# Kernel optimization log

Measured on AMD Instinct MI355X. Metric: run time of the kernel, lower is better.

Reference implementation:

```python
import jax, jax.numpy as jnp
import numpy as np

N_EMBD = 512
HEAD_SIZE = 64
B, T = 256, 256


def setup_inputs() -> dict:
    key = jax.random.key(0)
    ks = jax.random.split(key, 7)
    s = 1.0 / np.sqrt(N_EMBD)
    return {
        "x": jax.random.normal(ks[0], (B, T, N_EMBD), dtype=jnp.float32),
        "Wk": jax.random.uniform(ks[1], (N_EMBD, HEAD_SIZE), jnp.float32, -s, s),
        "bk": jax.random.uniform(ks[2], (HEAD_SIZE,), jnp.float32, -s, s),
        "Wq": jax.random.uniform(ks[3], (N_EMBD, HEAD_SIZE), jnp.float32, -s, s),
        "bq": jax.random.uniform(ks[4], (HEAD_SIZE,), jnp.float32, -s, s),
        "Wv": jax.random.uniform(ks[5], (N_EMBD, HEAD_SIZE), jnp.float32, -s, s),
        "bv": jax.random.uniform(ks[6], (HEAD_SIZE,), jnp.float32, -s, s),
    }


def reference(x, Wk, bk, Wq, bq, Wv, bv):
    # Single-head causal self-attention (dropout = identity in eval mode).
    Bq, Tq, C = x.shape
    k = x @ Wk + bk        # [B, T, H]
    q = x @ Wq + bq        # [B, T, H]
    v = x @ Wv + bv        # [B, T, H]
    scale = 1.0 / jnp.sqrt(jnp.asarray(k.shape[-1], x.dtype))
    scores = jnp.einsum('bth,bsh->bts', q, k) * scale  # [B, T, T]
    causal = jnp.tril(jnp.ones((Tq, Tq), dtype=bool))
    scores = jnp.where(causal, scores, -jnp.inf)
    attn = jax.nn.softmax(scores, axis=-1)
    return jnp.einsum('bts,bsh->bth', attn, v)  # [B, T, H]
```

## Files before the change

kernel.cpp:

```cpp
#include <hip/hip_runtime.h>
#include <stdint.h>

typedef __attribute__((ext_vector_type(8))) short bf16x8;
typedef __attribute__((ext_vector_type(4))) float f32x4;

#if __has_builtin(__builtin_amdgcn_exp2f)
#define EXP2F(x) __builtin_amdgcn_exp2f(x)
#else
#define EXP2F(x) exp2f(x)
#endif

__device__ __forceinline__ short f2bf(float f) {
    union { float f; uint32_t u; } c; c.f = f;
    return (short)((c.u + 0x7fffu + ((c.u >> 16) & 1u)) >> 16);
}

__global__ void prep_kernel(const float* __restrict__ Wk, const float* __restrict__ bk,
                            const float* __restrict__ Wq, const float* __restrict__ bq,
                            const float* __restrict__ Wv, const float* __restrict__ bv,
                            short* __restrict__ Wt2g, float* __restrict__ bcat) {
    const int col = blockIdx.x;
    const float* W; const float* bb; int c0;
    if (col < 64)       { W = Wk; bb = bk; c0 = col; }
    else if (col < 128) { W = Wq; bb = bq; c0 = col - 64; }
    else                { W = Wv; bb = bv; c0 = col - 128; }
    for (int c = threadIdx.x; c < 512; c += blockDim.x)
        Wt2g[(c >> 5) * (192 * 32) + col * 32 + (c & 31)] = f2bf(W[(size_t)c * 64 + c0]);
    if (threadIdx.x == 0) bcat[col] = bb[c0];
}

#define PSTR 40

__global__ __launch_bounds__(512, 2) void fused_kernel(
    const float* __restrict__ x, const short* __restrict__ Wt2g,
    const float* __restrict__ bcat, float* __restrict__ out) {
    extern __shared__ __align__(16) char smem[];
    short* Ks  = (short*)smem;
    short* Qs  = (short*)(smem + 32768);
    short* Vts = (short*)(smem + 65536);
    short* Ps  = (short*)(smem + 98304);

    const int tid = threadIdx.x;
    const int wave = tid >> 6, lane = tid & 63;
    const int quad = lane >> 4, l16 = lane & 15;
    const int b = blockIdx.x;
    const int ta = wave, tb = 15 - wave;

    f32x4 acc[2][12];
#pragma unroll
    for (int m = 0; m < 2; m++)
#pragma unroll
        for (int i = 0; i < 12; i++) acc[m][i] = (f32x4){0.f, 0.f, 0.f, 0.f};

    const float* xA0 = x + ((size_t)b * 256 + ta * 16 + l16) * 512 + quad * 8;
    const float* xA1 = x + ((size_t)b * 256 + tb * 16 + l16) * 512 + quad * 8;

    f32x4 p00 = *(const f32x4*)xA0, p01 = *(const f32x4*)(xA0 + 4);
    f32x4 p10 = *(const f32x4*)xA1, p11 = *(const f32x4*)(xA1 + 4);

    for (int kc = 0; kc < 16; kc++) {
        bf16x8 a0, a1;
#pragma unroll
        for (int i = 0; i < 4; i++) { a0[i] = f2bf(p00[i]); a0[4 + i] = f2bf(p01[i]); }
#pragma unroll
        for (int i = 0; i < 4; i++) { a1[i] = f2bf(p10[i]); a1[4 + i] = f2bf(p11[i]); }
        if (kc < 15) {
            p00 = *(const f32x4*)(xA0 + (kc + 1) * 32);
            p01 = *(const f32x4*)(xA0 + (kc + 1) * 32 + 4);
            p10 = *(const f32x4*)(xA1 + (kc + 1) * 32);
            p11 = *(const f32x4*)(xA1 + (kc + 1) * 32 + 4);
        }
        const short* wkc = Wt2g + kc * 6144 + l16 * 32 + quad * 8;
#pragma unroll
        for (int nt = 0; nt < 12; nt++) {
            bf16x8 bfrag = *(const bf16x8*)(wkc + nt * 512);
            acc[0][nt] = __builtin_amdgcn_mfma_f32_16x16x32_bf16(a0, bfrag, acc[0][nt], 0, 0, 0);
            acc[1][nt] = __builtin_amdgcn_mfma_f32_16x16x32_bf16(a1, bfrag, acc[1][nt], 0, 0, 0);
        }
    }

#pragma unroll
    for (int m = 0; m < 2; m++) {
        const int t = m ? tb : ta;
#pragma unroll
        for (int nt = 0; nt < 12; nt++) {
            const int col = nt * 16 + l16;
            const float bias = bcat[col];
            const int h = col & 63;
#pragma unroll
            for (int r = 0; r < 4; r++) {
                const short v = f2bf(acc[m][nt][r] + bias);
                const int row = t * 16 + quad * 4 + r;
                if (nt < 4)
                    Ks[row * 64 + (((h >> 3) ^ (row & 7)) << 3) + (h & 7)] = v;
                else if (nt < 8)
                    Qs[row * 64 + (((h >> 3) ^ (row & 7)) << 3) + (h & 7)] = v;
                else
                    Vts[h * 256 + (((row >> 3) ^ (h & 7)) << 3) + (row & 7)] = v;
            }
        }
    }
    __syncthreads();

    const float sc2 = 0.125f * 1.44269504088896340736f;
    short* myP = Ps + wave * (16 * PSTR);

#pragma unroll
    for (int ti = 0; ti < 2; ti++) {
        const int t = ti ? tb : ta;
        const int qrow = t * 16 + l16;
        const int sw = l16 & 7;
        bf16x8 qf0 = *(const bf16x8*)&Qs[qrow * 64 + ((quad ^ sw) << 3)];
        bf16x8 qf1 = *(const bf16x8*)&Qs[qrow * 64 + (((4 + quad) ^ sw) << 3)];

        f32x4 St[16];
#pragma unroll
        for (int i = 0; i < 16; i++) St[i] = (f32x4){0.f, 0.f, 0.f, 0.f};
#pragma unroll
        for (int nt = 0; nt < 16; nt++) if (nt <= t) {
            const int krow = nt * 16 + l16;
            bf16x8 kf0 = *(const bf16x8*)&Ks[krow * 64 + ((quad ^ sw) << 3)];
            bf16x8 kf1 = *(const bf16x8*)&Ks[krow * 64 + (((4 + quad) ^ sw) << 3)];
            St[nt] = __builtin_amdgcn_mfma_f32_16x16x32_bf16(qf0, kf0, St[nt], 0, 0, 0);
            St[nt] = __builtin_amdgcn_mfma_f32_16x16x32_bf16(qf1, kf1, St[nt], 0, 0, 0);
        }

        const int rowq = t * 16 + quad * 4;
        float mx[4], ls[4];
#pragma unroll
        for (int r = 0; r < 4; r++) mx[r] = -3.0e38f;
#pragma unroll
        for (int nt = 0; nt < 16; nt++) if (nt <= t) {
            const int cs = nt * 16 + l16;
#pragma unroll
            for (int r = 0; r < 4; r++) {
                float s = (cs <= rowq + r) ? St[nt][r] * sc2 : -3.0e38f;
                St[nt][r] = s;
                mx[r] = fmaxf(mx[r], s);
            }
        }
#pragma unroll
        for (int d = 1; d < 16; d <<= 1)
#pragma unroll
            for (int r = 0; r < 4; r++)
                mx[r] = fmaxf(mx[r], __shfl_xor(mx[r], d, 64));
#pragma unroll
        for (int r = 0; r < 4; r++) ls[r] = 0.f;
#pragma unroll
        for (int nt = 0; nt < 16; nt++) if (nt <= t) {
#pragma unroll
            for (int r = 0; r < 4; r++) {
                float p = EXP2F(St[nt][r] - mx[r]);
                St[nt][r] = p;
                ls[r] += p;
            }
        }
#pragma unroll
        for (int d = 1; d < 16; d <<= 1)
#pragma unroll
            for (int r = 0; r < 4; r++)
                ls[r] += __shfl_xor(ls[r], d, 64);

        f32x4 O[4];
#pragma unroll
        for (int i = 0; i < 4; i++) O[i] = (f32x4){0.f, 0.f, 0.f, 0.f};
        const int nch = (t + 2) >> 1;
#pragma unroll
        for (int c2 = 0; c2 < 8; c2++) if (c2 < nch) {
#pragma unroll
            for (int t2i = 0; t2i < 2; t2i++) {
                const int nt = c2 * 2 + t2i;
#pragma unroll
                for (int r = 0; r < 4; r++)
                    myP[(quad * 4 + r) * PSTR + t2i * 16 + l16] = f2bf(St[nt][r]);
            }
            bf16x8 pf = *(const bf16x8*)&myP[l16 * PSTR + quad * 8];
#pragma unroll
            for (int ht = 0; ht < 4; ht++) {
                const int h = ht * 16 + l16;
                bf16x8 vf = *(const bf16x8*)&Vts[h * 256 + ((((c2 * 4 + quad)) ^ (h & 7)) << 3)];
                O[ht] = __builtin_amdgcn_mfma_f32_16x16x32_bf16(pf, vf, O[ht], 0, 0, 0);
            }
        }

        float rls[4];
#pragma unroll
        for (int r = 0; r < 4; r++) rls[r] = 1.0f / ls[r];
#pragma unroll
        for (int ht = 0; ht < 4; ht++)
#pragma unroll
            for (int r = 0; r < 4; r++)
                out[((size_t)b * 256 + rowq + r) * 64 + ht * 16 + l16] = O[ht][r] * rls[r];
    }
}

extern "C" void kernel_launch(void* const* d_in, const int* in_sizes, int n_in,
                              void* d_out, int out_size, void* d_ws, size_t ws_size,
                              hipStream_t stream) {
    const float* x  = (const float*)d_in[0];
    const float* Wk = (const float*)d_in[1];
    const float* bk = (const float*)d_in[2];
    const float* Wq = (const float*)d_in[3];
    const float* bq = (const float*)d_in[4];
    const float* Wv = (const float*)d_in[5];
    const float* bv = (const float*)d_in[6];
    float* out = (float*)d_out;

    char* ws = (char*)d_ws;
    short* Wt2g = (short*)(ws);
    float* bcat = (float*)(ws + 196608);

    const int smem_bytes = 108544;
    (void)hipFuncSetAttribute((const void*)fused_kernel,
                              hipFuncAttributeMaxDynamicSharedMemorySize, smem_bytes);

    prep_kernel<<<192, 256, 0, stream>>>(Wk, bk, Wq, bq, Wv, bv, Wt2g, bcat);
    fused_kernel<<<256, 512, smem_bytes, stream>>>(x, Wt2g, bcat, out);
}
```

Baseline: 229.6 us.

## Stage x and W via async global-to-LDS double buffering with 16 waves

Moves the QKV projection operands into LDS with asynchronous global_load_lds copies, double-buffered across K chunks, and reads A and B fragments from shared memory instead of registers or global memory. The block grows to 1024 threads so each of 16 waves owns a single 16-row tile, replacing the paired balanced tiles per wave. This targets the latency of global loads in the projection phase. In exchange it adds extra LDS space and a barrier per K chunk, and causal work per wave becomes uneven in the attention phase.

```diff
diff --git a/kernel.cpp b/kernel.cpp
--- a/kernel.cpp
+++ b/kernel.cpp
@@ -13,6 +13,12 @@
 __device__ __forceinline__ short f2bf(float f) {
     union { float f; uint32_t u; } c; c.f = f;
     return (short)((c.u + 0x7fffu + ((c.u >> 16) & 1u)) >> 16);
+}
+
+typedef __attribute__((address_space(1))) void gvoid;
+typedef __attribute__((address_space(3))) void lvoid;
+__device__ __forceinline__ void async_cp16(const void* g, void* l) {
+    __builtin_amdgcn_global_load_lds((gvoid*)g, (lvoid*)l, 16, 0, 0);
 }
 
 __global__ void prep_kernel(const float* __restrict__ Wk, const float* __restrict__ bk,
@@ -31,73 +37,80 @@
 
 #define PSTR 40
 
-__global__ __launch_bounds__(512, 2) void fused_kernel(
+__global__ __launch_bounds__(1024, 4) void fused_kernel(
     const float* __restrict__ x, const short* __restrict__ Wt2g,
     const float* __restrict__ bcat, float* __restrict__ out) {
     extern __shared__ __align__(16) char smem[];
+
+    const int tid = threadIdx.x;
+    const int wave = tid >> 6, lane = tid & 63;
+    const int quad = lane >> 4, l16 = lane & 15;
+    const int b = blockIdx.x;
+    const int t = wave;
+
+    f32x4 acc[12];
+#pragma unroll
+    for (int i = 0; i < 12; i++) acc[i] = (f32x4){0.f, 0.f, 0.f, 0.f};
+
+    const int xr = lane >> 3;
+    const int xsl = lane & 7;
+
+#define STAGE_X(kc, bufp)                                                           \
+    for (int g = 0; g < 2; g++) {                                                   \
+        const int i = wave + g * 16;                                                \
+        const int r = i * 8 + xr;                                                   \
+        const int s = xsl ^ ((r & 3) << 1);                                         \
+        async_cp16(x + ((size_t)b * 256 + r) * 512 + (kc) * 32 + s * 4,             \
+                   smem + (bufp) * 32768 + i * 1024);                               \
+    }
+#define STAGE_W(kc, bufp)                                                           \
+    if (wave < 12) {                                                                \
+        async_cp16(Wt2g + (size_t)(kc) * 6144 + wave * 512 + lane * 8,              \
+                   smem + 65536 + (bufp) * 12288 + wave * 1024);                    \
+    }
+
+    STAGE_X(0, 0)
+    STAGE_W(0, 0)
+    __syncthreads();
+
+    const int axoff = (quad ^ (l16 & 3)) * 8;
+    const int arow = t * 16 + l16;
+    for (int kc = 0; kc < 16; kc++) {
+        const int buf = kc & 1;
+        if (kc < 15) { STAGE_X(kc + 1, buf ^ 1) STAGE_W(kc + 1, buf ^ 1) }
+        const float* xa = (const float*)(smem + buf * 32768) + arow * 32 + axoff;
+        f32x4 u0 = *(const f32x4*)xa, u1 = *(const f32x4*)(xa + 4);
+        bf16x8 a;
+#pragma unroll
+        for (int i = 0; i < 4; i++) { a[i] = f2bf(u0[i]); a[4 + i] = f2bf(u1[i]); }
+        const short* wb = (const short*)(smem + 65536 + buf * 12288);
+#pragma unroll
+        for (int nt = 0; nt < 12; nt++) {
+            bf16x8 bfrag = *(const bf16x8*)&wb[(nt * 16 + l16) * 32 + quad * 8];
+            acc[nt] = __builtin_amdgcn_mfma_f32_16x16x32_bf16(a, bfrag, acc[nt], 0, 0, 0);
+        }
+        __syncthreads();
+    }
+
     short* Ks  = (short*)smem;
     short* Qs  = (short*)(smem + 32768);
     short* Vts = (short*)(smem + 65536);
     short* Ps  = (short*)(smem + 98304);
-
-    const int tid = threadIdx.x;
-    const int wave = tid >> 6, lane = tid & 63;
-    const int quad = lane >> 4, l16 = lane & 15;
-    const int b = blockIdx.x;
-    const int ta = wave, tb = 15 - wave;
-
-    f32x4 acc[2][12];
-#pragma unroll
-    for (int m = 0; m < 2; m++)
-#pragma unroll
-        for (int i = 0; i < 12; i++) acc[m][i] = (f32x4){0.f, 0.f, 0.f, 0.f};
-
-    const float* xA0 = x + ((size_t)b * 256 + ta * 16 + l16) * 512 + quad * 8;
-    const float* xA1 = x + ((size_t)b * 256 + tb * 16 + l16) * 512 + quad * 8;
-
-    f32x4 p00 = *(const f32x4*)xA0, p01 = *(const f32x4*)(xA0 + 4);
-    f32x4 p10 = *(const f32x4*)xA1, p11 = *(const f32x4*)(xA1 + 4);
-
-    for (int kc = 0; kc < 16; kc++) {
-        bf16x8 a0, a1;
-#pragma unroll
-        for (int i = 0; i < 4; i++) { a0[i] = f2bf(p00[i]); a0[4 + i] = f2bf(p01[i]); }
-#pragma unroll
-        for (int i = 0; i < 4; i++) { a1[i] = f2bf(p10[i]); a1[4 + i] = f2bf(p11[i]); }
-        if (kc < 15) {
-            p00 = *(const f32x4*)(xA0 + (kc + 1) * 32);
-            p01 = *(const f32x4*)(xA0 + (kc + 1) * 32 + 4);
-            p10 = *(const f32x4*)(xA1 + (kc + 1) * 32);
-            p11 = *(const f32x4*)(xA1 + (kc + 1) * 32 + 4);
-        }
-        const short* wkc = Wt2g + kc * 6144 + l16 * 32 + quad * 8;
-#pragma unroll
-        for (int nt = 0; nt < 12; nt++) {
-            bf16x8 bfrag = *(const bf16x8*)(wkc + nt * 512);
-            acc[0][nt] = __builtin_amdgcn_mfma_f32_16x16x32_bf16(a0, bfrag, acc[0][nt], 0, 0, 0);
-            acc[1][nt] = __builtin_amdgcn_mfma_f32_16x16x32_bf16(a1, bfrag, acc[1][nt], 0, 0, 0);
-        }
-    }
-
-#pragma unroll
-    for (int m = 0; m < 2; m++) {
-        const int t = m ? tb : ta;
-#pragma unroll
-        for (int nt = 0; nt < 12; nt++) {
-            const int col = nt * 16 + l16;
-            const float bias = bcat[col];
-            const int h = col & 63;
-#pragma unroll
-            for (int r = 0; r < 4; r++) {
-                const short v = f2bf(acc[m][nt][r] + bias);
-                const int row = t * 16 + quad * 4 + r;
-                if (nt < 4)
-                    Ks[row * 64 + (((h >> 3) ^ (row & 7)) << 3) + (h & 7)] = v;
-                else if (nt < 8)
-                    Qs[row * 64 + (((h >> 3) ^ (row & 7)) << 3) + (h & 7)] = v;
-                else
-                    Vts[h * 256 + (((row >> 3) ^ (h & 7)) << 3) + (row & 7)] = v;
-            }
+#pragma unroll
+    for (int nt = 0; nt < 12; nt++) {
+        const int col = nt * 16 + l16;
+        const float bias = bcat[col];
+        const int h = col & 63;
+#pragma unroll
+        for (int r = 0; r < 4; r++) {
+            const short v = f2bf(acc[nt][r] + bias);
+            const int row = t * 16 + quad * 4 + r;
+            if (nt < 4)
+                Ks[row * 64 + (((h >> 3) ^ (row & 7)) << 3) + (h & 7)] = v;
+            else if (nt < 8)
+                Qs[row * 64 + (((h >> 3) ^ (row & 7)) << 3) + (h & 7)] = v;
+            else
+                Vts[h * 256 + (((row >> 3) ^ (h & 7)) << 3) + (row & 7)] = v;
         }
     }
     __syncthreads();
@@ -105,93 +118,91 @@
     const float sc2 = 0.125f * 1.44269504088896340736f;
     short* myP = Ps + wave * (16 * PSTR);
 
-#pragma unroll
-    for (int ti = 0; ti < 2; ti++) {
-        const int t = ti ? tb : ta;
-        const int qrow = t * 16 + l16;
-        const int sw = l16 & 7;
-        bf16x8 qf0 = *(const bf16x8*)&Qs[qrow * 64 + ((quad ^ sw) << 3)];
-        bf16x8 qf1 = *(const bf16x8*)&Qs[qrow * 64 + (((4 + quad) ^ sw) << 3)];
-
-        f32x4 St[16];
-#pragma unroll
-        for (int i = 0; i < 16; i++) St[i] = (f32x4){0.f, 0.f, 0.f, 0.f};
-#pragma unroll
-        for (int nt = 0; nt < 16; nt++) if (nt <= t) {
-            const int krow = nt * 16 + l16;
-            bf16x8 kf0 = *(const bf16x8*)&Ks[krow * 64 + ((quad ^ sw) << 3)];
-            bf16x8 kf1 = *(const bf16x8*)&Ks[krow * 64 + (((4 + quad) ^ sw) << 3)];
-            St[nt] = __builtin_amdgcn_mfma_f32_16x16x32_bf16(qf0, kf0, St[nt], 0, 0, 0);
-            St[nt] = __builtin_amdgcn_mfma_f32_16x16x32_bf16(qf1, kf1, St[nt], 0, 0, 0);
-        }
-
-        const int rowq = t * 16 + quad * 4;
-        float mx[4], ls[4];
-#pragma unroll
-        for (int r = 0; r < 4; r++) mx[r] = -3.0e38f;
-#pragma unroll
-        for (int nt = 0; nt < 16; nt++) if (nt <= t) {
-            const int cs = nt * 16 + l16;
-#pragma unroll
-            for (int r = 0; r < 4; r++) {
-                float s = (cs <= rowq + r) ? St[nt][r] * sc2 : -3.0e38f;
-                St[nt][r] = s;
-                mx[r] = fmaxf(mx[r], s);
-            }
-        }
-#pragma unroll
-        for (int d = 1; d < 16; d <<= 1)
+    const int qrow = t * 16 + l16;
+    const int sw = l16 & 7;
+    bf16x8 qf0 = *(const bf16x8*)&Qs[qrow * 64 + ((quad ^ sw) << 3)];
+    bf16x8 qf1 = *(const bf16x8*)&Qs[qrow * 64 + (((4 + quad) ^ sw) << 3)];
+
+    f32x4 St[16];
+#pragma unroll
+    for (int i = 0; i < 16; i++) St[i] = (f32x4){0.f, 0.f, 0.f, 0.f};
+#pragma unroll
+    for (int nt = 0; nt < 16; nt++) if (nt <= t) {
+        const int krow = nt * 16 + l16;
+        bf16x8 kf0 = *(const bf16x8*)&Ks[krow * 64 + ((quad ^ sw) << 3)];
+        bf16x8 kf1 = *(const bf16x8*)&Ks[krow * 64 + (((4 + quad) ^ sw) << 3)];
+        St[nt] = __builtin_amdgcn_mfma_f32_16x16x32_bf16(qf0, kf0, St[nt], 0, 0, 0);
+        St[nt] = __builtin_amdgcn_mfma_f32_16x16x32_bf16(qf1, kf1, St[nt], 0, 0, 0);
+    }
+
+    const int rowq = t * 16 + quad * 4;
+    float mx[4], ls[4];
+#pragma unroll
+    for (int r = 0; r < 4; r++) mx[r] = -3.0e38f;
+#pragma unroll
+    for (int nt = 0; nt < 16; nt++) if (nt <= t) {
+        const int cs = nt * 16 + l16;
+#pragma unroll
+        for (int r = 0; r < 4; r++) {
+            float s = (cs <= rowq + r) ? St[nt][r] * sc2 : -3.0e38f;
+            St[nt][r] = s;
+            mx[r] = fmaxf(mx[r], s);
+        }
+    }
+#pragma unroll
+    for (int d = 1; d < 16; d <<= 1)
+#pragma unroll
+        for (int r = 0; r < 4; r++)
+            mx[r] = fmaxf(mx[r], __shfl_xor(mx[r], d, 64));
+#pragma unroll
+    for (int r = 0; r < 4; r++) ls[r] = 0.f;
+#pragma unroll
+    for (int nt = 0; nt < 16; nt++) if (nt <= t) {
+#pragma unroll
+        for (int r = 0; r < 4; r++) {
+            float p = EXP2F(St[nt][r] - mx[r]);
+            St[nt][r] = p;
+            ls[r] += p;
+        }
+    }
+#pragma unroll
+    for (int d = 1; d < 16; d <<= 1)
+#pragma unroll
+        for (int r = 0; r < 4; r++)
+            ls[r] += __shfl_xor(ls[r], d, 64);
+
+    f32x4 O[4];
+#pragma unroll
+    for (int i = 0; i < 4; i++) O[i] = (f32x4){0.f, 0.f, 0.f, 0.f};
+    const int nch = (t + 2) >> 1;
+#pragma unroll
+    for (int c2 = 0; c2 < 8; c2++) if (c2 < nch) {
+#pragma unroll
+        for (int t2i = 0; t2i < 2; t2i++) {
+            const int nt = c2 * 2 + t2i;
 #pragma unroll
             for (int r = 0; r < 4; r++)
-                mx[r] = fmaxf(mx[r], __shfl_xor(mx[r], d, 64));
-#pragma unroll
-        for (int r = 0; r < 4; r++) ls[r] = 0.f;
-#pragma unroll
-        for (int nt = 0; nt < 16; nt++) if (nt <= t) {
-#pragma unroll
-            for (int r = 0; r < 4; r++) {
-                float p = EXP2F(St[nt][r] - mx[r]);
-                St[nt][r] = p;
-                ls[r] += p;
-            }
-        }
-#pragma unroll
-        for (int d = 1; d < 16; d <<= 1)
-#pragma unroll
-            for (int r = 0; r < 4; r++)
-                ls[r] += __shfl_xor(ls[r], d, 64);
-
-        f32x4 O[4];
-#pragma unroll
-        for (int i = 0; i < 4; i++) O[i] = (f32x4){0.f, 0.f, 0.f, 0.f};
-        const int nch = (t + 2) >> 1;
-#pragma unroll
-        for (int c2 = 0; c2 < 8; c2++) if (c2 < nch) {
-#pragma unroll
-            for (int t2i = 0; t2i < 2; t2i++) {
-                const int nt = c2 * 2 + t2i;
-#pragma unroll
-                for (int r = 0; r < 4; r++)
-                    myP[(quad * 4 + r) * PSTR + t2i * 16 + l16] = f2bf(St[nt][r]);
-            }
-            bf16x8 pf = *(const bf16x8*)&myP[l16 * PSTR + quad * 8];
-#pragma unroll
-            for (int ht = 0; ht < 4; ht++) {
-                const int h = ht * 16 + l16;
-                bf16x8 vf = *(const bf16x8*)&Vts[h * 256 + ((((c2 * 4 + quad)) ^ (h & 7)) << 3)];
-                O[ht] = __builtin_amdgcn_mfma_f32_16x16x32_bf16(pf, vf, O[ht], 0, 0, 0);
-            }
-        }
-
-        float rls[4];
-#pragma unroll
-        for (int r = 0; r < 4; r++) rls[r] = 1.0f / ls[r];
-#pragma unroll
-        for (int ht = 0; ht < 4; ht++)
-#pragma unroll
-            for (int r = 0; r < 4; r++)
-                out[((size_t)b * 256 + rowq + r) * 64 + ht * 16 + l16] = O[ht][r] * rls[r];
-    }
+                myP[(quad * 4 + r) * PSTR + t2i * 16 + l16] = f2bf(St[nt][r]);
+        }
+        bf16x8 pf = *(const bf16x8*)&myP[l16 * PSTR + quad * 8];
+#pragma unroll
+        for (int ht = 0; ht < 4; ht++) {
+            const int h = ht * 16 + l16;
+            bf16x8 vf = *(const bf16x8*)&Vts[h * 256 + (((c2 * 4 + quad) ^ (h & 7)) << 3)];
+            O[ht] = __builtin_amdgcn_mfma_f32_16x16x32_bf16(pf, vf, O[ht], 0, 0, 0);
+        }
+    }
+
+    float rls[4];
+#pragma unroll
+    for (int r = 0; r < 4; r++) rls[r] = 1.0f / ls[r];
+#pragma unroll
+    for (int ht = 0; ht < 4; ht++)
+#pragma unroll
+        for (int r = 0; r < 4; r++)
+            out[((size_t)b * 256 + rowq + r) * 64 + ht * 16 + l16] = O[ht][r] * rls[r];
+#undef STAGE_X
+#undef STAGE_W
 }
 
 extern "C" void kernel_launch(void* const* d_in, const int* in_sizes, int n_in,
@@ -210,10 +221,10 @@
     short* Wt2g = (short*)(ws);
     float* bcat = (float*)(ws + 196608);
 
-    const int smem_bytes = 108544;
+    const int smem_bytes = 118784;
     (void)hipFuncSetAttribute((const void*)fused_kernel,
                               hipFuncAttributeMaxDynamicSharedMemorySize, smem_bytes);
 
     prep_kernel<<<192, 256, 0, stream>>>(Wk, bk, Wq, bq, Wv, bv, Wt2g, bcat);
-    fused_kernel<<<256, 512, smem_bytes, stream>>>(x, Wt2g, bcat, out);
-}
+    fused_kernel<<<256, 1024, smem_bytes, stream>>>(x, Wt2g, bcat, out);
+}
```

Result: faster. 217.1 us (-5.5%).
